# Performance work log

Hardware: AMD Instinct MI355X
Metric: run time of the kernel (lower is better)

## Reference

```python
import jax, jax.numpy as jnp
import numpy as np

COST_CLASS = 1.0
COST_BBOX = 5.0
COST_GIOU = 2.0
BS, NQ, NC, M = 16, 1000, 92, 1024


def box_cxcywh_to_xyxy(x):
    xc, yc, w, h = jnp.split(x, 4, axis=-1)
    return jnp.concatenate([xc - 0.5 * w, yc - 0.5 * h, xc + 0.5 * w, yc + 0.5 * h], axis=-1)


def generalized_box_iou(a, b):
    # a: [N,4] xyxy, b: [M,4] xyxy -> [N,M]
    area_a = (a[:, 2] - a[:, 0]) * (a[:, 3] - a[:, 1])
    area_b = (b[:, 2] - b[:, 0]) * (b[:, 3] - b[:, 1])
    lt = jnp.maximum(a[:, None, :2], b[None, :, :2])  # [N,M,2]
    rb = jnp.minimum(a[:, None, 2:], b[None, :, 2:])
    wh = jnp.clip(rb - lt, 0.0)
    inter = wh[..., 0] * wh[..., 1]
    union = area_a[:, None] + area_b[None, :] - inter
    iou = inter / union
    lt_e = jnp.minimum(a[:, None, :2], b[None, :, :2])
    rb_e = jnp.maximum(a[:, None, 2:], b[None, :, 2:])
    wh_e = jnp.clip(rb_e - lt_e, 0.0)
    area_e = wh_e[..., 0] * wh_e[..., 1]
    return iou - (area_e - union) / area_e


def setup_inputs() -> dict:
    key = jax.random.key(0)
    k1, k2, k3, k4 = jax.random.split(key, 4)
    return {
        'pred_logits': jax.random.normal(k1, (BS, NQ, NC), dtype=jnp.float32),
        'pred_boxes': jax.random.uniform(k2, (BS, NQ, 4), dtype=jnp.float32),
        'tgt_boxes': jax.random.uniform(k3, (M, 4), dtype=jnp.float32),
        'tgt_labels': jax.random.randint(k4, (M,), 0, NC),
    }


def reference(pred_logits, pred_boxes, tgt_boxes, tgt_labels):
    bs, nq, nc = pred_logits.shape
    out_prob = jax.nn.softmax(pred_logits.reshape(bs * nq, nc), axis=-1)
    out_bbox = pred_boxes.reshape(bs * nq, 4)
    tgt_ids = jnp.clip(tgt_labels, 0, nc - 1)
    # classification cost: -prob of target class, gathered per target -> [N, M]
    cost_class = -out_prob[:, tgt_ids]
    # L1 cdist on cxcywh boxes -> [N, M]
    cost_bbox = jnp.abs(out_bbox[:, None, :] - tgt_bbox_b(tgt_boxes)[None, :, :]).sum(-1)
    cost_giou = -generalized_box_iou(box_cxcywh_to_xyxy(out_bbox), box_cxcywh_to_xyxy(tgt_boxes))
    C = COST_BBOX * cost_bbox + COST_CLASS * cost_class + COST_GIOU * cost_giou
    return C.reshape(bs, nq, -1)


def tgt_bbox_b(tgt_boxes):
    return tgt_boxes
```

## Files before the change

kernel.cpp:

```cpp
#include <hip/hip_runtime.h>
#include <math.h>


#define NROWS 16000
#define NC 92
#define M_TGT 1024
#define TPB 256
#define ROWS 16
#define KPT 4

__global__ __launch_bounds__(TPB) void hungarian_cost_kernel(
    const float* __restrict__ logits,
    const float* __restrict__ pboxes,
    const float* __restrict__ tboxes,
    const int*   __restrict__ tlabels,
    float* __restrict__ out)
{
    const int n0 = blockIdx.x * ROWS;
    const int t = threadIdx.x;
    const int lane = t & 63;
    const int wid  = t >> 6;

    __shared__ float negp[ROWS][NC];

    #pragma unroll
    for (int j = 0; j < 4; ++j) {
        const int r = wid * 4 + j;
        const float* lg = logits + (size_t)(n0 + r) * NC;
        const float x0 = lg[lane];
        const bool  hi = (lane < NC - 64);
        const float x1 = hi ? lg[64 + lane] : -INFINITY;
        float mx = fmaxf(x0, x1);
        #pragma unroll
        for (int off = 32; off >= 1; off >>= 1)
            mx = fmaxf(mx, __shfl_xor(mx, off));
        const float e0 = __expf(x0 - mx);
        const float e1 = hi ? __expf(x1 - mx) : 0.0f;
        float s = e0 + e1;
        #pragma unroll
        for (int off = 32; off >= 1; off >>= 1)
            s += __shfl_xor(s, off);
        const float rs = __builtin_amdgcn_rcpf(s);
        negp[r][lane] = fmaf(-e0, rs, 2.0f);
        if (hi) negp[r][64 + lane] = fmaf(-e1, rs, 2.0f);
    }

    float tcx[KPT], tcy[KPT], twd[KPT], tht[KPT];
    float bx0[KPT], by0[KPT], bx1[KPT], by1[KPT], areab[KPT];
    const int4 lb4 = reinterpret_cast<const int4*>(tlabels)[t];
    int lbl[KPT] = {lb4.x, lb4.y, lb4.z, lb4.w};
    #pragma unroll
    for (int k = 0; k < KPT; ++k) {
        const float4 tb = reinterpret_cast<const float4*>(tboxes)[4 * t + k];
        tcx[k] = tb.x; tcy[k] = tb.y; twd[k] = tb.z; tht[k] = tb.w;
        bx0[k] = fmaf(-0.5f, tb.z, tb.x);  by0[k] = fmaf(-0.5f, tb.w, tb.y);
        bx1[k] = fmaf( 0.5f, tb.z, tb.x);  by1[k] = fmaf( 0.5f, tb.w, tb.y);
        areab[k] = tb.z * tb.w;
        lbl[k] = (lbl[k] < 0) ? 0 : (lbl[k] > NC - 1 ? NC - 1 : lbl[k]);
    }
    __syncthreads();

    #pragma unroll 4
    for (int r = 0; r < ROWS; ++r) {
        const float4 pb = reinterpret_cast<const float4*>(pboxes)[n0 + r];
        const float ax0 = fmaf(-0.5f, pb.z, pb.x);
        const float ay0 = fmaf(-0.5f, pb.w, pb.y);
        const float ax1 = fmaf( 0.5f, pb.z, pb.x);
        const float ay1 = fmaf( 0.5f, pb.w, pb.y);
        const float area_a = pb.z * pb.w;
        const float* __restrict__ np = negp[r];

        float tmp[KPT];
        #pragma unroll
        for (int k = 0; k < KPT; ++k) {
            const float cls2 = np[lbl[k]];
            const float cb = fabsf(pb.x - tcx[k]) + fabsf(pb.y - tcy[k])
                           + fabsf(pb.z - twd[k]) + fabsf(pb.w - tht[k]);
            const float iwu = fminf(ax1, bx1[k]) - fmaxf(ax0, bx0[k]);
            const float ihu = fminf(ay1, by1[k]) - fmaxf(ay0, by0[k]);
            const float inter = fmaxf(iwu, 0.0f) * fmaxf(ihu, 0.0f);
            const float uni = area_a + areab[k] - inter;
            const float ew = pb.z + twd[k] - iwu;
            const float eh = pb.w + tht[k] - ihu;
            const float ae = ew * eh;
            const float h = fmaf(inter, __builtin_amdgcn_rcpf(uni),
                                 uni * __builtin_amdgcn_rcpf(ae));
            tmp[k] = fmaf(5.0f, cb, cls2) - 2.0f * h;
        }
        float4 res = {tmp[0], tmp[1], tmp[2], tmp[3]};
        reinterpret_cast<float4*>(out + ((size_t)(n0 + r) << 10))[t] = res;
    }
}

extern "C" void kernel_launch(void* const* d_in, const int* in_sizes, int n_in,
                              void* d_out, int out_size, void* d_ws, size_t ws_size,
                              hipStream_t stream) {
    const float* logits  = (const float*)d_in[0];
    const float* pboxes  = (const float*)d_in[1];
    const float* tboxes  = (const float*)d_in[2];
    const int*   tlabels = (const int*)d_in[3];
    float* out = (float*)d_out;

    hungarian_cost_kernel<<<NROWS / ROWS, TPB, 0, stream>>>(
        logits, pboxes, tboxes, tlabels, out);
}
```

Measured before the change: 26.42 us.

## Split softmax into separate kernel and use persistent grid-stride cost kernel

```diff
diff --git a/kernel.cpp b/kernel.cpp
--- a/kernel.cpp
+++ b/kernel.cpp
@@ -6,23 +6,104 @@
 #define NC 92
 #define M_TGT 1024
 #define TPB 256
-#define ROWS 16
 #define KPT 4
+#define GRID_B 2000
 
-__global__ __launch_bounds__(TPB) void hungarian_cost_kernel(
+typedef float f32x4 __attribute__((ext_vector_type(4)));
+
+__global__ __launch_bounds__(TPB) void softmax_p2_kernel(
     const float* __restrict__ logits,
+    float* __restrict__ p2)
+{
+    const int lane = threadIdx.x & 63;
+    const int row  = blockIdx.x * 4 + (threadIdx.x >> 6);
+    const float* lg = logits + (size_t)row * NC;
+    const float x0 = lg[lane];
+    const bool  hi = (lane < NC - 64);
+    const float x1 = hi ? lg[64 + lane] : -INFINITY;
+    float mx = fmaxf(x0, x1);
+    #pragma unroll
+    for (int off = 32; off >= 1; off >>= 1)
+        mx = fmaxf(mx, __shfl_xor(mx, off));
+    const float e0 = __expf(x0 - mx);
+    const float e1 = hi ? __expf(x1 - mx) : 0.0f;
+    float s = e0 + e1;
+    #pragma unroll
+    for (int off = 32; off >= 1; off >>= 1)
+        s += __shfl_xor(s, off);
+    const float rs = __builtin_amdgcn_rcpf(s);
+    float* pr = p2 + (size_t)row * NC;
+    pr[lane] = fmaf(-e0, rs, 2.0f);
+    if (hi) pr[64 + lane] = fmaf(-e1, rs, 2.0f);
+}
+
+__global__ __launch_bounds__(TPB) void cost_kernel(
+    const float* __restrict__ p2,
     const float* __restrict__ pboxes,
     const float* __restrict__ tboxes,
     const int*   __restrict__ tlabels,
+    float* __restrict__ out)
+{
+    const int t = threadIdx.x;
+
+    float tcx[KPT], tcy[KPT], twd[KPT], tht[KPT];
+    float bx0[KPT], by0[KPT], bx1[KPT], by1[KPT], areab[KPT];
+    const int4 lb4 = reinterpret_cast<const int4*>(tlabels)[t];
+    int lbl[KPT] = {lb4.x, lb4.y, lb4.z, lb4.w};
+    #pragma unroll
+    for (int k = 0; k < KPT; ++k) {
+        const float4 tb = reinterpret_cast<const float4*>(tboxes)[4 * t + k];
+        tcx[k] = tb.x; tcy[k] = tb.y; twd[k] = tb.z; tht[k] = tb.w;
+        bx0[k] = fmaf(-0.5f, tb.z, tb.x);  by0[k] = fmaf(-0.5f, tb.w, tb.y);
+        bx1[k] = fmaf( 0.5f, tb.z, tb.x);  by1[k] = fmaf( 0.5f, tb.w, tb.y);
+        areab[k] = tb.z * tb.w;
+        lbl[k] = (lbl[k] < 0) ? 0 : (lbl[k] > NC - 1 ? NC - 1 : lbl[k]);
+    }
+
+    #pragma unroll 2
+    for (int n = blockIdx.x; n < NROWS; n += GRID_B) {
+        const float4 pb = reinterpret_cast<const float4*>(pboxes)[n];
+        const float ax0 = fmaf(-0.5f, pb.z, pb.x);
+        const float ay0 = fmaf(-0.5f, pb.w, pb.y);
+        const float ax1 = fmaf( 0.5f, pb.z, pb.x);
+        const float ay1 = fmaf( 0.5f, pb.w, pb.y);
+        const float area_a = pb.z * pb.w;
+        const float* __restrict__ pr = p2 + (size_t)n * NC;
+
+        float tmp[KPT];
+        #pragma unroll
+        for (int k = 0; k < KPT; ++k) {
+            const float cls2 = pr[lbl[k]];
+            const float cb = fabsf(pb.x - tcx[k]) + fabsf(pb.y - tcy[k])
+                           + fabsf(pb.z - twd[k]) + fabsf(pb.w - tht[k]);
+            const float iwu = fminf(ax1, bx1[k]) - fmaxf(ax0, bx0[k]);
+            const float ihu = fminf(ay1, by1[k]) - fmaxf(ay0, by0[k]);
+            const float inter = fmaxf(iwu, 0.0f) * fmaxf(ihu, 0.0f);
+            const float uni = area_a + areab[k] - inter;
+            const float ew = pb.z + twd[k] - iwu;
+            const float eh = pb.w + tht[k] - ihu;
+            const float ae = ew * eh;
+            const float h = fmaf(inter, __builtin_amdgcn_rcpf(uni),
+                                 uni * __builtin_amdgcn_rcpf(ae));
+            tmp[k] = fmaf(5.0f, cb, cls2) - 2.0f * h;
+        }
+        f32x4 res = {tmp[0], tmp[1], tmp[2], tmp[3]};
+        __builtin_nontemporal_store(res,
+            reinterpret_cast<f32x4*>(out + ((size_t)n << 10)) + t);
+    }
+}
+
+#define ROWS 16
+__global__ __launch_bounds__(TPB) void hungarian_mono_kernel(
+    const float* __restrict__ logits, const float* __restrict__ pboxes,
+    const float* __restrict__ tboxes, const int* __restrict__ tlabels,
     float* __restrict__ out)
 {
     const int n0 = blockIdx.x * ROWS;
     const int t = threadIdx.x;
     const int lane = t & 63;
     const int wid  = t >> 6;
-
     __shared__ float negp[ROWS][NC];
-
     #pragma unroll
     for (int j = 0; j < 4; ++j) {
         const int r = wid * 4 + j;
@@ -44,7 +125,6 @@
         negp[r][lane] = fmaf(-e0, rs, 2.0f);
         if (hi) negp[r][64 + lane] = fmaf(-e1, rs, 2.0f);
     }
-
     float tcx[KPT], tcy[KPT], twd[KPT], tht[KPT];
     float bx0[KPT], by0[KPT], bx1[KPT], by1[KPT], areab[KPT];
     const int4 lb4 = reinterpret_cast<const int4*>(tlabels)[t];
@@ -59,7 +139,6 @@
         lbl[k] = (lbl[k] < 0) ? 0 : (lbl[k] > NC - 1 ? NC - 1 : lbl[k]);
     }
     __syncthreads();
-
     #pragma unroll 4
     for (int r = 0; r < ROWS; ++r) {
         const float4 pb = reinterpret_cast<const float4*>(pboxes)[n0 + r];
@@ -69,7 +148,6 @@
         const float ay1 = fmaf( 0.5f, pb.w, pb.y);
         const float area_a = pb.z * pb.w;
         const float* __restrict__ np = negp[r];
-
         float tmp[KPT];
         #pragma unroll
         for (int k = 0; k < KPT; ++k) {
@@ -101,6 +179,13 @@
     const int*   tlabels = (const int*)d_in[3];
     float* out = (float*)d_out;
 
-    hungarian_cost_kernel<<<NROWS / ROWS, TPB, 0, stream>>>(
-        logits, pboxes, tboxes, tlabels, out);
+    const size_t p2_bytes = (size_t)NROWS * NC * sizeof(float);
+    if (ws_size >= p2_bytes) {
+        float* p2 = (float*)d_ws;
+        softmax_p2_kernel<<<NROWS / 4, TPB, 0, stream>>>(logits, p2);
+        cost_kernel<<<GRID_B, TPB, 0, stream>>>(p2, pboxes, tboxes, tlabels, out);
+    } else {
+        hungarian_mono_kernel<<<NROWS / ROWS, TPB, 0, stream>>>(
+            logits, pboxes, tboxes, tlabels, out);
+    }
 }
```

Result: slower. 28.39 us (+7.4%).
